# Kernel tuning notes

Hardware: AMD Instinct MI355X
Metric: run time of the kernel (lower is better)

## Reference

```python
import jax, jax.numpy as jnp
import numpy as np

B, N, D = 2, 256, 512
H = 4 * D  # mlp_hidden_dim


def setup_inputs() -> dict:
    key = jax.random.key(0)
    ks = jax.random.split(key, 14)
    s_in = 1.0 / np.sqrt(D)
    s_h = 1.0 / np.sqrt(H)
    s_cat = 1.0 / np.sqrt(2 * D)
    return {
        "x_v": jax.random.normal(ks[0], (B, N, D), jnp.float32),
        "x_a": jax.random.normal(ks[1], (B, N, D), jnp.float32),
        # weights stored as (in, out); y = x @ W + b (same math as torch Linear)
        "W1v": jax.random.uniform(ks[2], (D, H), jnp.float32, -s_in, s_in),
        "b1v": jax.random.uniform(ks[3], (H,), jnp.float32, -s_in, s_in),
        "W1a": jax.random.uniform(ks[4], (D, H), jnp.float32, -s_in, s_in),
        "b1a": jax.random.uniform(ks[5], (H,), jnp.float32, -s_in, s_in),
        "Wmv": jax.random.uniform(ks[6], (H, D), jnp.float32, -s_h, s_h),
        "bmv": jax.random.uniform(ks[7], (D,), jnp.float32, -s_h, s_h),
        "Wma": jax.random.uniform(ks[8], (H, D), jnp.float32, -s_h, s_h),
        "bma": jax.random.uniform(ks[9], (D,), jnp.float32, -s_h, s_h),
        "Wout": jax.random.uniform(ks[10], (2 * D, D), jnp.float32, -s_cat, s_cat),
        "bout": jax.random.uniform(ks[11], (D,), jnp.float32, -s_cat, s_cat),
    }


def reference(x_v, x_a, W1v, b1v, W1a, b1a, Wmv, bmv, Wma, bma, Wout, bout):
    # pairwise Manhattan distance: [B, N, M]
    dist = jnp.sum(jnp.abs(x_v[:, :, None, :] - x_a[:, None, :, :]), axis=-1)
    dv = dist.mean(axis=2)  # [B, N] mean distance of each v-token to all a-tokens
    da = dist.mean(axis=1)  # [B, M]
    xv_w = x_v * dv[..., None]
    xa_w = x_a * da[..., None]
    # dropout prob = 0.0 -> identity
    hv = jax.nn.gelu(xv_w @ W1v + b1v, approximate=False) @ Wmv + bmv
    ha = jax.nn.gelu(xa_w @ W1a + b1a, approximate=False) @ Wma + bma
    combined = jnp.concatenate([hv, ha], axis=-1)  # [B, N, 2D]
    return combined @ Wout + bout
```

## Files before the change

kernel.cpp:

```cpp
#include <hip/hip_runtime.h>
#include <math.h>

#define Bsz  2
#define Ntok 256
#define Ddim 512
#define Hdim 2048
#define Mrows 512

typedef __bf16 bf16_8 __attribute__((ext_vector_type(8)));
typedef __bf16 bf16_4 __attribute__((ext_vector_type(4)));
typedef __bf16 bf16_2 __attribute__((ext_vector_type(2)));
typedef float  f32x4_t __attribute__((ext_vector_type(4)));

struct PrepPtrs {
    const float* src[3];
    __bf16*      dst[3];
    const float* xv;
    const float* xa;
    __bf16*      xbf[2];
    float*       pv;
    float*       pa;
    const float* bm[2];
    const float* Wout;
    const float* bout;
    float*       bc;
};

__global__ __launch_bounds__(256) void prep_kernel(PrepPtrs p) {
    __shared__ float tile[64][65];
    __shared__ float red[4][4];

    int blk = blockIdx.x;
    int tid = threadIdx.x;

    if (blk < 640) {
        const int Ks[3]  = {512, 512, 1024};
        const int Ns[3]  = {2048, 2048, 512};
        const int off[4] = {0, 256, 512, 640};
        int mi = 0;
        while (blk >= off[mi + 1]) ++mi;
        int local = blk - off[mi];
        int shift = (mi < 2) ? 5 : 3;
        int bx = local & ((1 << shift) - 1);
        int by = local >> shift;
        const float* src = p.src[mi];
        __bf16*      dst = p.dst[mi];
        int K = Ks[mi], N = Ns[mi];
        int n0 = bx << 6, k0 = by << 6;

        int klb = tid >> 4, nl = (tid & 15) << 2;
#pragma unroll
        for (int pass = 0; pass < 4; ++pass) {
            int kl = (pass << 4) + klb;
            float4 v = *(const float4*)&src[(size_t)(k0 + kl) * N + n0 + nl];
            tile[kl][nl + 0] = v.x;
            tile[kl][nl + 1] = v.y;
            tile[kl][nl + 2] = v.z;
            tile[kl][nl + 3] = v.w;
        }
        __syncthreads();
        int nl2 = tid >> 2, kb = (tid & 3) << 2;
#pragma unroll
        for (int pass = 0; pass < 4; ++pass) {
            int kl2 = (pass << 4) + kb;
            bf16_4 o;
#pragma unroll
            for (int i = 0; i < 4; ++i) o[i] = (__bf16)tile[kl2 + i][nl2];
            *(bf16_4*)&dst[(size_t)(n0 + nl2) * K + k0 + kl2] = o;
        }
    } else if (blk < 1664) {
        int bx   = blk - 640;
        int jc   = bx & 3;
        int g    = bx >> 2;
        int role = g >> 7;
        int b    = (g >> 6) & 1;
        int i0   = (g & 63) << 2;
        const float* Q    = role ? p.xa : p.xv;
        const float* S    = role ? p.xv : p.xa;
        float*       outp = role ? p.pa : p.pv;

        int d0 = tid << 1;
        const float* Qb = Q + ((size_t)b * Ntok + i0) * Ddim + d0;
        const float* Sb = S + ((size_t)b * Ntok + (jc << 6)) * Ddim + d0;

        float2 q[4];
#pragma unroll
        for (int r = 0; r < 4; ++r) q[r] = *(const float2*)(Qb + r * Ddim);

        if (jc == 0) {
            __bf16* xb = p.xbf[role];
#pragma unroll
            for (int r = 0; r < 4; ++r) {
                bf16_2 o;
                o[0] = (__bf16)q[r].x;
                o[1] = (__bf16)q[r].y;
                *(bf16_2*)&xb[((size_t)b * Ntok + i0 + r) * Ddim + d0] = o;
            }
        }

        float acc[4] = {0.f, 0.f, 0.f, 0.f};
#pragma unroll 4
        for (int j = 0; j < 64; ++j) {
            float2 s = *(const float2*)(Sb + (size_t)j * Ddim);
#pragma unroll
            for (int r = 0; r < 4; ++r)
                acc[r] += fabsf(q[r].x - s.x) + fabsf(q[r].y - s.y);
        }
        int lane = tid & 63, wv = tid >> 6;
#pragma unroll
        for (int r = 0; r < 4; ++r) {
            float v = acc[r];
#pragma unroll
            for (int off2 = 32; off2; off2 >>= 1) v += __shfl_down(v, off2);
            if (lane == 0) red[wv][r] = v;
        }
        __syncthreads();
        if (tid < 4) {
            float v = red[0][tid] + red[1][tid] + red[2][tid] + red[3][tid];
            outp[jc * Mrows + b * Ntok + i0 + tid] = v;
        }
    } else {
        int kb = blk - 1664;
        float a0 = 0.f, a1 = 0.f, a2 = 0.f, a3 = 0.f;
#pragma unroll 4
        for (int kk = 0; kk < 128; kk += 2) {
            int k0 = (kb << 7) + kk, k1 = k0 + 1;
            float bk0 = (k0 < 512) ? p.bm[0][k0] : p.bm[1][k0 - 512];
            float bk1 = (k1 < 512) ? p.bm[0][k1] : p.bm[1][k1 - 512];
            a0 += bk0 * p.Wout[(size_t)k0 * Ddim + tid];
            a1 += bk0 * p.Wout[(size_t)k0 * Ddim + tid + 256];
            a2 += bk1 * p.Wout[(size_t)k1 * Ddim + tid];
            a3 += bk1 * p.Wout[(size_t)k1 * Ddim + tid + 256];
        }
        if (kb == 0) { a0 += p.bout[tid]; a1 += p.bout[tid + 256]; }
        atomicAdd(&p.bc[tid],       a0 + a2);
        atomicAdd(&p.bc[tid + 256], a1 + a3);
    }
}

template <int GELU, int AMODE, int BFP32, int OUTM>
__device__ void gemm_tile(__bf16 (&As)[2][64][40], __bf16 (&Bs)[2][64][40],
                          const void* Aa, int lda, const void* Bv, int ldb,
                          const float* bias, const float* scale4,
                          void* C, int ldc, int Kdim,
                          int m0, int n0, int addBias) {
    const int tid = threadIdx.x;
    const int row = tid >> 2;
    const int kc  = (tid & 3) << 3;

    const __bf16* Bb  = (const __bf16*)Bv + (size_t)(n0 + row) * ldb + kc;
    const float*  Bf  = (const float*)Bv + (size_t)(n0 + row) * ldb + kc;
    const float*  Af  = (const float*)Aa + (size_t)(m0 + row) * lda + kc;
    const __bf16* Ab  = (const __bf16*)Aa + (size_t)(m0 + row) * lda + kc;
    float s = 1.0f;
    if (AMODE == 1 || AMODE == 3) {
        int m = m0 + row;
        s = (scale4[m] + scale4[Mrows + m] + scale4[2 * Mrows + m] +
             scale4[3 * Mrows + m]) * (1.0f / 256.0f);
    }

    const int wave = tid >> 6, lane = tid & 63;
    const int moff = (wave >> 1) << 5, noff = (wave & 1) << 5;
    const int lrow = lane & 15, quad = lane >> 4;

    struct Stage {
        float4 aF0, aF1, bF0, bF1;
        bf16_8 a8, b8;
    };
    Stage sR, sN;

    auto loadStage = [&](int kt, Stage& st) {
        if (BFP32) {
            st.bF0 = *(const float4*)(Bf + kt);
            st.bF1 = *(const float4*)(Bf + kt + 4);
        } else {
            st.b8 = *(const bf16_8*)(Bb + kt);
        }
        if (AMODE == 1) {
            st.aF0 = *(const float4*)(Af + kt);
            st.aF1 = *(const float4*)(Af + kt + 4);
        } else {
            st.a8 = *(const bf16_8*)(Ab + kt);
        }
    };
    auto storeStage = [&](int buf, const Stage& st) {
        bf16_8 a8, b8;
        if (AMODE == 1) {
            a8[0] = (__bf16)(st.aF0.x * s); a8[1] = (__bf16)(st.aF0.y * s);
            a8[2] = (__bf16)(st.aF0.z * s); a8[3] = (__bf16)(st.aF0.w * s);
            a8[4] = (__bf16)(st.aF1.x * s); a8[5] = (__bf16)(st.aF1.y * s);
            a8[6] = (__bf16)(st.aF1.z * s); a8[7] = (__bf16)(st.aF1.w * s);
        } else if (AMODE == 3) {
#pragma unroll
            for (int i = 0; i < 8; ++i)
                a8[i] = (__bf16)((float)st.a8[i] * s);
        } else {
            a8 = st.a8;
        }
        if (BFP32) {
            b8[0] = (__bf16)st.bF0.x; b8[1] = (__bf16)st.bF0.y;
            b8[2] = (__bf16)st.bF0.z; b8[3] = (__bf16)st.bF0.w;
            b8[4] = (__bf16)st.bF1.x; b8[5] = (__bf16)st.bF1.y;
            b8[6] = (__bf16)st.bF1.z; b8[7] = (__bf16)st.bF1.w;
        } else {
            b8 = st.b8;
        }
        *(bf16_8*)&As[buf][row][kc] = a8;
        *(bf16_8*)&Bs[buf][row][kc] = b8;
    };

    f32x4_t acc00 = {0.f, 0.f, 0.f, 0.f};
    f32x4_t acc01 = {0.f, 0.f, 0.f, 0.f};
    f32x4_t acc10 = {0.f, 0.f, 0.f, 0.f};
    f32x4_t acc11 = {0.f, 0.f, 0.f, 0.f};

    const int nIter = Kdim >> 5;

    loadStage(0, sR);
    storeStage(0, sR);
    if (nIter > 1) loadStage(32, sR);
    __syncthreads();

    for (int it = 0; it < nIter; ++it) {
        const int cur = it & 1;
        bf16_8 a0 = *(const bf16_8*)&As[cur][moff + lrow][quad << 3];
        bf16_8 a1 = *(const bf16_8*)&As[cur][moff + 16 + lrow][quad << 3];
        bf16_8 b0 = *(const bf16_8*)&Bs[cur][noff + lrow][quad << 3];
        bf16_8 b1 = *(const bf16_8*)&Bs[cur][noff + 16 + lrow][quad << 3];
        if (it + 2 < nIter) loadStage((it + 2) << 5, sN);
        acc00 = __builtin_amdgcn_mfma_f32_16x16x32_bf16(a0, b0, acc00, 0, 0, 0);
        acc01 = __builtin_amdgcn_mfma_f32_16x16x32_bf16(a0, b1, acc01, 0, 0, 0);
        acc10 = __builtin_amdgcn_mfma_f32_16x16x32_bf16(a1, b0, acc10, 0, 0, 0);
        acc11 = __builtin_amdgcn_mfma_f32_16x16x32_bf16(a1, b1, acc11, 0, 0, 0);
        if (it + 1 < nIter) {
            storeStage(cur ^ 1, sR);
            sR = sN;
            __syncthreads();
        }
    }

    f32x4_t accs[2][2] = {{acc00, acc01}, {acc10, acc11}};
#pragma unroll
    for (int ti = 0; ti < 2; ++ti) {
#pragma unroll
        for (int tj = 0; tj < 2; ++tj) {
            int colg = n0 + noff + (tj << 4) + lrow;
            float bv = addBias ? bias[colg] : 0.0f;
#pragma unroll
            for (int r = 0; r < 4; ++r) {
                int rowg = m0 + moff + (ti << 4) + (quad << 2) + r;
                float v = accs[ti][tj][r] + bv;
                if (GELU) v = 0.5f * v * (1.0f + erff(v * 0.70710678118654752f));
                if (OUTM == 1)
                    ((__bf16*)C)[(size_t)rowg * ldc + colg] = (__bf16)v;
                else
                    atomicAdd((float*)C + (size_t)rowg * ldc + colg, v);
            }
        }
    }
}

struct APtrs {
    const __bf16* xbf[2];
    const __bf16* WT1[2];
    const float*  b1[2];
    const float*  pd[2];
    __bf16*       g1[2];
    const __bf16* WTout;
    const float*  Wm[2];
    __bf16*       WcT[2];
};

__global__ __launch_bounds__(256) void kernelA(APtrs p) {
    __shared__ __align__(16) __bf16 As[2][64][40];
    __shared__ __align__(16) __bf16 Bs[2][64][40];
    int blk = blockIdx.x;
    if (blk < 512) {
        int z = blk >> 8, t = blk & 255;
        int mt = t >> 5, nt = t & 31;
        gemm_tile<1, 3, 0, 1>(As, Bs, p.xbf[z], Ddim, p.WT1[z], Ddim,
                              p.b1[z], p.pd[z], p.g1[z], Hdim, Ddim,
                              mt << 6, nt << 6, 1);
    } else {
        int b2 = blk - 512;
        int z = b2 >> 8, t = b2 & 255;
        int mt = t >> 5, nt = t & 31;
        gemm_tile<0, 0, 1, 1>(As, Bs, p.WTout + z * 512, 2 * Ddim,
                              p.Wm[z], Ddim, nullptr, nullptr,
                              p.WcT[z], Hdim, Ddim, mt << 6, nt << 6, 0);
    }
}

struct BPtrs {
    const __bf16* g1[2];
    const __bf16* WcT[2];
    const float*  bc;
    float*        out;
};

__global__ __launch_bounds__(256) void kernelB(BPtrs p) {
    __shared__ __align__(16) __bf16 As[2][64][40];
    __shared__ __align__(16) __bf16 Bs[2][64][40];
    int nt = blockIdx.x & 7, mt = (blockIdx.x >> 3) & 7, kz = blockIdx.x >> 6;
    int z = kz >> 2, koff = (kz & 3) << 9;
    gemm_tile<0, 0, 0, 2>(As, Bs, p.g1[z] + koff, Hdim, p.WcT[z] + koff, Hdim,
                          p.bc, nullptr, p.out, Ddim, Ddim,
                          mt << 6, nt << 6, kz == 0);
}

extern "C" void kernel_launch(void* const* d_in, const int* in_sizes, int n_in,
                              void* d_out, int out_size, void* d_ws, size_t ws_size,
                              hipStream_t stream) {
    const float* x_v  = (const float*)d_in[0];
    const float* x_a  = (const float*)d_in[1];
    const float* W1v  = (const float*)d_in[2];
    const float* b1v  = (const float*)d_in[3];
    const float* W1a  = (const float*)d_in[4];
    const float* b1a  = (const float*)d_in[5];
    const float* Wmv  = (const float*)d_in[6];
    const float* bmv  = (const float*)d_in[7];
    const float* Wma  = (const float*)d_in[8];
    const float* bma  = (const float*)d_in[9];
    const float* Wout = (const float*)d_in[10];
    const float* bout = (const float*)d_in[11];
    float* out = (float*)d_out;

    char* w = (char*)d_ws;
    auto alloc = [&](size_t bytes) {
        char* r = w;
        w += (bytes + 255) & ~(size_t)255;
        return (void*)r;
    };
    float*    pv    = (float*)alloc(4 * Mrows * 4);
    float*    pa    = (float*)alloc(4 * Mrows * 4);
    float*    bc    = (float*)alloc(Ddim * 4);
    __bf16*   xbfv  = (__bf16*)alloc((size_t)Mrows * Ddim * 2);
    __bf16*   xbfa  = (__bf16*)alloc((size_t)Mrows * Ddim * 2);
    __bf16*   WT1v  = (__bf16*)alloc((size_t)Hdim * Ddim * 2);
    __bf16*   WT1a  = (__bf16*)alloc((size_t)Hdim * Ddim * 2);
    __bf16*   WTout = (__bf16*)alloc((size_t)Ddim * 2 * Ddim * 2);
    __bf16*   WcTv  = (__bf16*)alloc((size_t)Ddim * Hdim * 2);
    __bf16*   WcTa  = (__bf16*)alloc((size_t)Ddim * Hdim * 2);
    __bf16*   g1v   = (__bf16*)alloc((size_t)Mrows * Hdim * 2);
    __bf16*   g1a   = (__bf16*)alloc((size_t)Mrows * Hdim * 2);

    hipMemsetAsync(out, 0, (size_t)Mrows * Ddim * 4, stream);
    hipMemsetAsync(bc, 0, Ddim * 4, stream);

    PrepPtrs pp;
    pp.src[0] = W1v;  pp.dst[0] = WT1v;
    pp.src[1] = W1a;  pp.dst[1] = WT1a;
    pp.src[2] = Wout; pp.dst[2] = WTout;
    pp.xv = x_v; pp.xa = x_a;
    pp.xbf[0] = xbfv; pp.xbf[1] = xbfa;
    pp.pv = pv; pp.pa = pa;
    pp.bm[0] = bmv; pp.bm[1] = bma;
    pp.Wout = Wout; pp.bout = bout;
    pp.bc = bc;
    prep_kernel<<<dim3(1672), dim3(256), 0, stream>>>(pp);

    APtrs ap;
    ap.xbf[0] = xbfv; ap.xbf[1] = xbfa;
    ap.WT1[0] = WT1v; ap.WT1[1] = WT1a;
    ap.b1[0] = b1v; ap.b1[1] = b1a;
    ap.pd[0] = pv; ap.pd[1] = pa;
    ap.g1[0] = g1v; ap.g1[1] = g1a;
    ap.WTout = WTout;
    ap.Wm[0] = Wmv; ap.Wm[1] = Wma;
    ap.WcT[0] = WcTv; ap.WcT[1] = WcTa;
    kernelA<<<dim3(1024), dim3(256), 0, stream>>>(ap);

    BPtrs bp;
    bp.g1[0] = g1v; bp.g1[1] = g1a;
    bp.WcT[0] = WcTv; bp.WcT[1] = WcTa;
    bp.bc = bc; bp.out = out;
    kernelB<<<dim3(512), dim3(256), 0, stream>>>(bp);
}
```

Before: 129.5 us.

## Widen GEMM tiles to 64x128 and fold memsets into prep kernel

```diff
diff --git a/kernel.cpp b/kernel.cpp
--- a/kernel.cpp
+++ b/kernel.cpp
@@ -24,6 +24,7 @@
     const float* Wout;
     const float* bout;
     float*       bc;
+    float*       outz;
 };
 
 __global__ __launch_bounds__(256) void prep_kernel(PrepPtrs p) {
@@ -119,7 +120,7 @@
             float v = red[0][tid] + red[1][tid] + red[2][tid] + red[3][tid];
             outp[jc * Mrows + b * Ntok + i0 + tid] = v;
         }
-    } else {
+    } else if (blk < 1672) {
         int kb = blk - 1664;
         float a0 = 0.f, a1 = 0.f, a2 = 0.f, a3 = 0.f;
 #pragma unroll 4
@@ -133,39 +134,51 @@
             a3 += bk1 * p.Wout[(size_t)k1 * Ddim + tid + 256];
         }
         if (kb == 0) { a0 += p.bout[tid]; a1 += p.bout[tid + 256]; }
-        atomicAdd(&p.bc[tid],       a0 + a2);
-        atomicAdd(&p.bc[tid + 256], a1 + a3);
+        p.bc[(kb << 9) + tid]       = a0 + a2;
+        p.bc[(kb << 9) + tid + 256] = a1 + a3;
+    } else {
+        int ib = blk - 1672;
+        float4 z4 = {0.f, 0.f, 0.f, 0.f};
+        float4* o = (float4*)p.outz + (size_t)ib * 1024 + tid;
+#pragma unroll
+        for (int pass = 0; pass < 4; ++pass) o[pass * 256] = z4;
     }
 }
 
 template <int GELU, int AMODE, int BFP32, int OUTM>
-__device__ void gemm_tile(__bf16 (&As)[2][64][40], __bf16 (&Bs)[2][64][40],
+__device__ void gemm_tile(__bf16 (&As)[2][64][40], __bf16 (&Bs)[2][128][40],
                           const void* Aa, int lda, const void* Bv, int ldb,
                           const float* bias, const float* scale4,
                           void* C, int ldc, int Kdim,
                           int m0, int n0, int addBias) {
     const int tid = threadIdx.x;
-    const int row = tid >> 2;
-    const int kc  = (tid & 3) << 3;
-
-    const __bf16* Bb  = (const __bf16*)Bv + (size_t)(n0 + row) * ldb + kc;
-    const float*  Bf  = (const float*)Bv + (size_t)(n0 + row) * ldb + kc;
-    const float*  Af  = (const float*)Aa + (size_t)(m0 + row) * lda + kc;
-    const __bf16* Ab  = (const __bf16*)Aa + (size_t)(m0 + row) * lda + kc;
+    const int arow = tid >> 2;
+    const int akc  = (tid & 3) << 3;
+    const int brow = tid >> 1;
+    const int bkc  = (tid & 1) << 4;
+
+    const __bf16* Ab = (const __bf16*)Aa + (size_t)(m0 + arow) * lda + akc;
+    const float*  Af = (const float*) Aa + (size_t)(m0 + arow) * lda + akc;
+    const __bf16* Bb = (const __bf16*)Bv + (size_t)(n0 + brow) * ldb + bkc;
+    const float*  Bf = (const float*) Bv + (size_t)(n0 + brow) * ldb + bkc;
+
     float s = 1.0f;
     if (AMODE == 1 || AMODE == 3) {
-        int m = m0 + row;
+        int m = m0 + arow;
         s = (scale4[m] + scale4[Mrows + m] + scale4[2 * Mrows + m] +
              scale4[3 * Mrows + m]) * (1.0f / 256.0f);
     }
 
     const int wave = tid >> 6, lane = tid & 63;
-    const int moff = (wave >> 1) << 5, noff = (wave & 1) << 5;
+    const int moff = (wave >> 1) << 5;
+    const int noff = (wave & 1) << 6;
     const int lrow = lane & 15, quad = lane >> 4;
 
     struct Stage {
-        float4 aF0, aF1, bF0, bF1;
-        bf16_8 a8, b8;
+        float4 aF0, aF1;
+        float4 bF0, bF1, bF2, bF3;
+        bf16_8 a8;
+        bf16_8 b8a, b8b;
     };
     Stage sR, sN;
 
@@ -173,8 +186,11 @@
         if (BFP32) {
             st.bF0 = *(const float4*)(Bf + kt);
             st.bF1 = *(const float4*)(Bf + kt + 4);
+            st.bF2 = *(const float4*)(Bf + kt + 8);
+            st.bF3 = *(const float4*)(Bf + kt + 12);
         } else {
-            st.b8 = *(const bf16_8*)(Bb + kt);
+            st.b8a = *(const bf16_8*)(Bb + kt);
+            st.b8b = *(const bf16_8*)(Bb + kt + 8);
         }
         if (AMODE == 1) {
             st.aF0 = *(const float4*)(Af + kt);
@@ -184,7 +200,7 @@
         }
     };
     auto storeStage = [&](int buf, const Stage& st) {
-        bf16_8 a8, b8;
+        bf16_8 a8;
         if (AMODE == 1) {
             a8[0] = (__bf16)(st.aF0.x * s); a8[1] = (__bf16)(st.aF0.y * s);
             a8[2] = (__bf16)(st.aF0.z * s); a8[3] = (__bf16)(st.aF0.w * s);
@@ -197,22 +213,31 @@
         } else {
             a8 = st.a8;
         }
+        bf16_8 b8a, b8b;
         if (BFP32) {
-            b8[0] = (__bf16)st.bF0.x; b8[1] = (__bf16)st.bF0.y;
-            b8[2] = (__bf16)st.bF0.z; b8[3] = (__bf16)st.bF0.w;
-            b8[4] = (__bf16)st.bF1.x; b8[5] = (__bf16)st.bF1.y;
-            b8[6] = (__bf16)st.bF1.z; b8[7] = (__bf16)st.bF1.w;
+            b8a[0] = (__bf16)st.bF0.x; b8a[1] = (__bf16)st.bF0.y;
+            b8a[2] = (__bf16)st.bF0.z; b8a[3] = (__bf16)st.bF0.w;
+            b8a[4] = (__bf16)st.bF1.x; b8a[5] = (__bf16)st.bF1.y;
+            b8a[6] = (__bf16)st.bF1.z; b8a[7] = (__bf16)st.bF1.w;
+            b8b[0] = (__bf16)st.bF2.x; b8b[1] = (__bf16)st.bF2.y;
+            b8b[2] = (__bf16)st.bF2.z; b8b[3] = (__bf16)st.bF2.w;
+            b8b[4] = (__bf16)st.bF3.x; b8b[5] = (__bf16)st.bF3.y;
+            b8b[6] = (__bf16)st.bF3.z; b8b[7] = (__bf16)st.bF3.w;
         } else {
-            b8 = st.b8;
-        }
-        *(bf16_8*)&As[buf][row][kc] = a8;
-        *(bf16_8*)&Bs[buf][row][kc] = b8;
+            b8a = st.b8a;
+            b8b = st.b8b;
+        }
+        *(bf16_8*)&As[buf][arow][akc] = a8;
+        *(bf16_8*)&Bs[buf][brow][bkc]     = b8a;
+        *(bf16_8*)&Bs[buf][brow][bkc + 8] = b8b;
     };
 
-    f32x4_t acc00 = {0.f, 0.f, 0.f, 0.f};
-    f32x4_t acc01 = {0.f, 0.f, 0.f, 0.f};
-    f32x4_t acc10 = {0.f, 0.f, 0.f, 0.f};
-    f32x4_t acc11 = {0.f, 0.f, 0.f, 0.f};
+    f32x4_t acc0[4], acc1[4];
+#pragma unroll
+    for (int j = 0; j < 4; ++j) {
+        acc0[j] = {0.f, 0.f, 0.f, 0.f};
+        acc1[j] = {0.f, 0.f, 0.f, 0.f};
+    }
 
     const int nIter = Kdim >> 5;
 
@@ -225,13 +250,16 @@
         const int cur = it & 1;
         bf16_8 a0 = *(const bf16_8*)&As[cur][moff + lrow][quad << 3];
         bf16_8 a1 = *(const bf16_8*)&As[cur][moff + 16 + lrow][quad << 3];
-        bf16_8 b0 = *(const bf16_8*)&Bs[cur][noff + lrow][quad << 3];
-        bf16_8 b1 = *(const bf16_8*)&Bs[cur][noff + 16 + lrow][quad << 3];
+        bf16_8 b[4];
+#pragma unroll
+        for (int j = 0; j < 4; ++j)
+            b[j] = *(const bf16_8*)&Bs[cur][noff + (j << 4) + lrow][quad << 3];
         if (it + 2 < nIter) loadStage((it + 2) << 5, sN);
-        acc00 = __builtin_amdgcn_mfma_f32_16x16x32_bf16(a0, b0, acc00, 0, 0, 0);
-        acc01 = __builtin_amdgcn_mfma_f32_16x16x32_bf16(a0, b1, acc01, 0, 0, 0);
-        acc10 = __builtin_amdgcn_mfma_f32_16x16x32_bf16(a1, b0, acc10, 0, 0, 0);
-        acc11 = __builtin_amdgcn_mfma_f32_16x16x32_bf16(a1, b1, acc11, 0, 0, 0);
+#pragma unroll
+        for (int j = 0; j < 4; ++j) {
+            acc0[j] = __builtin_amdgcn_mfma_f32_16x16x32_bf16(a0, b[j], acc0[j], 0, 0, 0);
+            acc1[j] = __builtin_amdgcn_mfma_f32_16x16x32_bf16(a1, b[j], acc1[j], 0, 0, 0);
+        }
         if (it + 1 < nIter) {
             storeStage(cur ^ 1, sR);
             sR = sN;
@@ -239,17 +267,23 @@
         }
     }
 
-    f32x4_t accs[2][2] = {{acc00, acc01}, {acc10, acc11}};
 #pragma unroll
     for (int ti = 0; ti < 2; ++ti) {
 #pragma unroll
-        for (int tj = 0; tj < 2; ++tj) {
+        for (int tj = 0; tj < 4; ++tj) {
             int colg = n0 + noff + (tj << 4) + lrow;
-            float bv = addBias ? bias[colg] : 0.0f;
+            float bv = 0.0f;
+            if (addBias == 1) {
+                bv = bias[colg];
+            } else if (addBias == 2) {
+#pragma unroll
+                for (int k = 0; k < 8; ++k) bv += bias[(k << 9) + colg];
+            }
+            f32x4_t av = ti ? acc1[tj] : acc0[tj];
 #pragma unroll
             for (int r = 0; r < 4; ++r) {
                 int rowg = m0 + moff + (ti << 4) + (quad << 2) + r;
-                float v = accs[ti][tj][r] + bv;
+                float v = av[r] + bv;
                 if (GELU) v = 0.5f * v * (1.0f + erff(v * 0.70710678118654752f));
                 if (OUTM == 1)
                     ((__bf16*)C)[(size_t)rowg * ldc + colg] = (__bf16)v;
@@ -273,21 +307,21 @@
 
 __global__ __launch_bounds__(256) void kernelA(APtrs p) {
     __shared__ __align__(16) __bf16 As[2][64][40];
-    __shared__ __align__(16) __bf16 Bs[2][64][40];
+    __shared__ __align__(16) __bf16 Bs[2][128][40];
     int blk = blockIdx.x;
-    if (blk < 512) {
-        int z = blk >> 8, t = blk & 255;
-        int mt = t >> 5, nt = t & 31;
+    if (blk < 256) {
+        int z = blk >> 7, t = blk & 127;
+        int mt = t >> 4, nt = t & 15;
         gemm_tile<1, 3, 0, 1>(As, Bs, p.xbf[z], Ddim, p.WT1[z], Ddim,
                               p.b1[z], p.pd[z], p.g1[z], Hdim, Ddim,
-                              mt << 6, nt << 6, 1);
+                              mt << 6, nt << 7, 1);
     } else {
-        int b2 = blk - 512;
-        int z = b2 >> 8, t = b2 & 255;
-        int mt = t >> 5, nt = t & 31;
+        int b2 = blk - 256;
+        int z = b2 >> 7, t = b2 & 127;
+        int mt = t >> 4, nt = t & 15;
         gemm_tile<0, 0, 1, 1>(As, Bs, p.WTout + z * 512, 2 * Ddim,
                               p.Wm[z], Ddim, nullptr, nullptr,
-                              p.WcT[z], Hdim, Ddim, mt << 6, nt << 6, 0);
+                              p.WcT[z], Hdim, Ddim, mt << 6, nt << 7, 0);
     }
 }
 
@@ -300,12 +334,12 @@
 
 __global__ __launch_bounds__(256) void kernelB(BPtrs p) {
     __shared__ __align__(16) __bf16 As[2][64][40];
-    __shared__ __align__(16) __bf16 Bs[2][64][40];
-    int nt = blockIdx.x & 7, mt = (blockIdx.x >> 3) & 7, kz = blockIdx.x >> 6;
+    __shared__ __align__(16) __bf16 Bs[2][128][40];
+    int nt = blockIdx.x & 3, mt = (blockIdx.x >> 2) & 7, kz = blockIdx.x >> 5;
     int z = kz >> 2, koff = (kz & 3) << 9;
     gemm_tile<0, 0, 0, 2>(As, Bs, p.g1[z] + koff, Hdim, p.WcT[z] + koff, Hdim,
                           p.bc, nullptr, p.out, Ddim, Ddim,
-                          mt << 6, nt << 6, kz == 0);
+                          mt << 6, nt << 7, kz == 0 ? 2 : 0);
 }
 
 extern "C" void kernel_launch(void* const* d_in, const int* in_sizes, int n_in,
@@ -333,7 +367,7 @@
     };
     float*    pv    = (float*)alloc(4 * Mrows * 4);
     float*    pa    = (float*)alloc(4 * Mrows * 4);
-    float*    bc    = (float*)alloc(Ddim * 4);
+    float*    bc    = (float*)alloc(8 * Ddim * 4);
     __bf16*   xbfv  = (__bf16*)alloc((size_t)Mrows * Ddim * 2);
     __bf16*   xbfa  = (__bf16*)alloc((size_t)Mrows * Ddim * 2);
     __bf16*   WT1v  = (__bf16*)alloc((size_t)Hdim * Ddim * 2);
@@ -343,9 +377,6 @@
     __bf16*   WcTa  = (__bf16*)alloc((size_t)Ddim * Hdim * 2);
     __bf16*   g1v   = (__bf16*)alloc((size_t)Mrows * Hdim * 2);
     __bf16*   g1a   = (__bf16*)alloc((size_t)Mrows * Hdim * 2);
-
-    hipMemsetAsync(out, 0, (size_t)Mrows * Ddim * 4, stream);
-    hipMemsetAsync(bc, 0, Ddim * 4, stream);
 
     PrepPtrs pp;
     pp.src[0] = W1v;  pp.dst[0] = WT1v;
@@ -357,7 +388,8 @@
     pp.bm[0] = bmv; pp.bm[1] = bma;
     pp.Wout = Wout; pp.bout = bout;
     pp.bc = bc;
-    prep_kernel<<<dim3(1672), dim3(256), 0, stream>>>(pp);
+    pp.outz = out;
+    prep_kernel<<<dim3(1736), dim3(256), 0, stream>>>(pp);
 
     APtrs ap;
     ap.xbf[0] = xbfv; ap.xbf[1] = xbfa;
@@ -368,11 +400,11 @@
     ap.WTout = WTout;
     ap.Wm[0] = Wmv; ap.Wm[1] = Wma;
     ap.WcT[0] = WcTv; ap.WcT[1] = WcTa;
-    kernelA<<<dim3(1024), dim3(256), 0, stream>>>(ap);
+    kernelA<<<dim3(512), dim3(256), 0, stream>>>(ap);
 
     BPtrs bp;
     bp.g1[0] = g1v; bp.g1[1] = g1a;
     bp.WcT[0] = WcTv; bp.WcT[1] = WcTa;
     bp.bc = bc; bp.out = out;
-    kernelB<<<dim3(512), dim3(256), 0, stream>>>(bp);
+    kernelB<<<dim3(256), dim3(256), 0, stream>>>(bp);
 }
```

Result: no change. 131.7 us (+1.7%).
